# Kernel optimization log

Measured on AMD Instinct MI355X. Metric: run time of the kernel, lower is better.

## Reference

```python
import jax, jax.numpy as jnp
import numpy as np

N = 50000
E = 800000
FEAT = 128
HID = 128
HEADS = 8
HEAD_DIM = HID // HEADS  # 16
NEG_SLOPE = 0.2


def _gat_layer(x, W, a_src, a_dst, b, src, dst, num_nodes):
    # x: [N, Fin]; W: [Fin, H*C]; a_src/a_dst: [H, C]; b: [H*C]
    H, C = a_src.shape
    h = (x @ W).reshape(num_nodes, H, C)               # [N,H,C]
    alpha_s = jnp.einsum('nhc,hc->nh', h, a_src)       # [N,H]
    alpha_d = jnp.einsum('nhc,hc->nh', h, a_dst)       # [N,H]
    e = jax.nn.leaky_relu(alpha_s[src] + alpha_d[dst], NEG_SLOPE)  # [E,H]
    # segment softmax over destination nodes (every node has a self-loop)
    m = jax.ops.segment_max(e, dst, num_segments=num_nodes)
    e = jnp.exp(e - m[dst])
    s = jax.ops.segment_sum(e, dst, num_segments=num_nodes)
    alpha = e / (s[dst] + 1e-16)                       # [E,H]
    msg = alpha[:, :, None] * h[src]                   # [E,H,C]
    out = jax.ops.segment_sum(msg, dst, num_segments=num_nodes)
    return out.reshape(num_nodes, H * C) + b


def setup_inputs() -> dict:
    key = jax.random.key(0)
    ks = jax.random.split(key, 12)
    x = jax.random.normal(ks[0], (N, FEAT), dtype=jnp.float32)
    edge_index = jax.random.randint(ks[1], (2, E), 0, N, dtype=jnp.int32)
    glorot = lambda k, shape: jax.random.uniform(
        k, shape, jnp.float32,
        -jnp.sqrt(6.0 / (shape[-2] + shape[-1])),
        jnp.sqrt(6.0 / (shape[-2] + shape[-1])))
    W1 = glorot(ks[2], (FEAT, HID))
    a_src1 = glorot(ks[3], (HEADS, HEAD_DIM))
    a_dst1 = glorot(ks[4], (HEADS, HEAD_DIM))
    b1 = jnp.zeros((HID,), jnp.float32)
    W2 = glorot(ks[5], (HID, HID))
    a_src2 = glorot(ks[6], (HEADS, HEAD_DIM))
    a_dst2 = glorot(ks[7], (HEADS, HEAD_DIM))
    b2 = jnp.zeros((HID,), jnp.float32)
    return {"x": x, "edge_index": edge_index,
            "W1": W1, "a_src1": a_src1, "a_dst1": a_dst1, "b1": b1,
            "W2": W2, "a_src2": a_src2, "a_dst2": a_dst2, "b2": b2}


def reference(x, edge_index, W1, a_src1, a_dst1, b1, W2, a_src2, a_dst2, b2):
    # GATConv adds self-loops to the (dense_to_sparse-derived) edge list
    loops = jnp.arange(N, dtype=edge_index.dtype)
    src = jnp.concatenate([edge_index[0], loops])
    dst = jnp.concatenate([edge_index[1], loops])
    h = _gat_layer(x, W1, a_src1, a_dst1, b1, src, dst, N)
    h = jax.nn.elu(h)
    # dropout: inference mode (training=False) -> identity
    h = _gat_layer(h, W2, a_src2, a_dst2, b2, src, dst, N)
    return jax.nn.elu(h)
```

## Files before the change

### kernel.cpp

```cpp
#include <hip/hip_runtime.h>
#include <hip/hip_fp16.h>
#include <math.h>

#define DEGMAX 64
#define CHUNK  2048
#define CAPB   6144
#define HCAP   (CAPB / 2)

typedef _Float16 half8 __attribute__((ext_vector_type(8)));
typedef float    f32x4 __attribute__((ext_vector_type(4)));

__global__ __launch_bounds__(256) void k_csr(
        const int* __restrict__ gcur, const unsigned* __restrict__ bstore,
        int N, int* __restrict__ cnt, unsigned short* __restrict__ adjt) {
    int blk = blockIdx.x;
    int b = blk >> 1, hh = blk & 1;
    int n0 = b * 256 + hh * 128;
    int nb = N - n0; if (nb > 128) nb = 128; if (nb < 0) nb = 0;
    int ecnt = gcur[b * 16]; if (ecnt > CAPB) ecnt = CAPB;
    const unsigned* bp = bstore + (size_t)b * CAPB;
    __shared__ int lcnt[128], lofs[128], wsum[2];
    __shared__ unsigned short stage[HCAP];
    int t = threadIdx.x;
    int lo = hh * 128;

    if (t < 128) lcnt[t] = 0;
    __syncthreads();
    for (int i = t; i < ecnt; i += 256) {
        int node = bp[i] >> 16;
        if ((node >> 7) == hh) atomicAdd(&lcnt[node - lo], 1);
    }
    __syncthreads();
    int mycnt = (t < 128) ? lcnt[t] : 0;
    int lane = t & 63, wv = t >> 6;
    int x = mycnt;
    #pragma unroll
    for (int d = 1; d < 64; d <<= 1) {
        int y = __shfl_up(x, d);
        if (lane >= d) x += y;
    }
    if (lane == 63 && wv < 2) wsum[wv] = x;
    __syncthreads();
    int base0 = (wv == 1) ? wsum[0] : 0;
    int myofs = base0 + x - mycnt;
    if (t < 128) lofs[t] = myofs;
    if (t < nb) cnt[n0 + t] = mycnt;
    __syncthreads();
    if (t < 128) lcnt[t] = 0;
    __syncthreads();
    for (int i = t; i < ecnt; i += 256) {
        unsigned p = bp[i];
        int node = p >> 16;
        if ((node >> 7) == hh) {
            int ln = node - lo;
            int r = atomicAdd(&lcnt[ln], 1);
            int pos = lofs[ln] + r;
            if (pos < HCAP) stage[pos] = (unsigned short)(p & 0xffffu);
        }
    }
    __syncthreads();
    for (int ln = wv; ln < 128; ln += 4) {
        int node = n0 + ln;
        if (node < N) {
            int c = lcnt[ln]; if (c > DEGMAX) c = DEGMAX;
            int p = lofs[ln] + lane;
            if (lane < c && p < HCAP)
                *(unsigned short*)((char*)adjt + (size_t)node * 128 + lane * 2) = stage[p];
        }
    }
}

__global__ void k_wcast(const float* __restrict__ W1, const float* __restrict__ as1,
                        const float* __restrict__ ad1, __half* __restrict__ Wf1,
                        const float* __restrict__ W2, const float* __restrict__ as2,
                        const float* __restrict__ ad2, __half* __restrict__ Wf2,
                        int* __restrict__ gcur) {
    int t = threadIdx.x;
    int id2 = blockIdx.x * 256 + t;
    if (id2 < 4096) gcur[id2] = 0;
    if (id2 >= 4608) return;
    int layer = id2 >= 2304 ? 1 : 0;
    const float* W  = layer ? W2  : W1;
    const float* av_s = layer ? as2 : as1;
    const float* av_d = layer ? ad2 : ad1;
    __half* Wf = layer ? Wf2 : Wf1;
    int id = id2 - layer * 2304;
    int lane = id & 63;
    int ct = (id >> 6) % 9;
    int kc = id / 576;
    int q = lane >> 4, n = lane & 15;
    #pragma unroll
    for (int j = 0; j < 8; j++) {
        int k = kc * 32 + q * 8 + j;
        float val;
        if (ct < 8) {
            val = W[(size_t)k * 128 + ct * 16 + n];
        } else {
            int h = n & 7;
            const float* a = (n < 8) ? av_s : av_d;
            float s = 0.f;
            #pragma unroll
            for (int c = 0; c < 16; c++)
                s += W[(size_t)k * 128 + h * 16 + c] * a[h * 16 + c];
            val = s;
        }
        Wf[(size_t)id * 8 + j] = __float2half(val);
    }
}

__device__ inline float4 ld4f(const float* p) { return *(const float4*)p; }

template<typename InT>
__device__ __forceinline__ void gemm_body(
        const InT* __restrict__ X, const __half* __restrict__ Wfrag,
        __half* __restrict__ H16, float* __restrict__ as_out,
        float* __restrict__ ad_out, int M, int bid) {
    __shared__ __half xls[64][136];
    int t = threadIdx.x;
    int w = t >> 6, lane = t & 63;
    int q = lane >> 4, n = lane & 15;
    int row0 = bid * 64;

    half8 bfrag[4][2];
    #pragma unroll
    for (int kc = 0; kc < 4; kc++)
        #pragma unroll
        for (int c2 = 0; c2 < 2; c2++) {
            int ct = w * 2 + c2;
            uint4 u = *(const uint4*)(Wfrag + (((size_t)(kc * 9 + ct)) * 64 + lane) * 8);
            bfrag[kc][c2] = *(half8*)&u;
        }
    half8 bfa[4];
    if (w == 0) {
        #pragma unroll
        for (int kc = 0; kc < 4; kc++) {
            uint4 u = *(const uint4*)(Wfrag + (((size_t)(kc * 9 + 8)) * 64 + lane) * 8);
            bfa[kc] = *(half8*)&u;
        }
    }

    #pragma unroll
    for (int rep = 0; rep < 8; rep++) {
        int lin = rep * 1024 + t * 4;
        int r = lin >> 7, k = lin & 127;
        int gr = row0 + r;
        uint2 u;
        if constexpr (sizeof(InT) == 4) {
            float4 v = (gr < M) ? ld4f((const float*)&X[(size_t)gr * 128 + k])
                                : make_float4(0.f, 0.f, 0.f, 0.f);
            __half2 h0 = __floats2half2_rn(v.x, v.y);
            __half2 h1 = __floats2half2_rn(v.z, v.w);
            u = make_uint2(*(unsigned*)&h0, *(unsigned*)&h1);
        } else {
            u = (gr < M) ? *(const uint2*)&X[(size_t)gr * 128 + k] : make_uint2(0, 0);
        }
        *(uint2*)&xls[r][k] = u;
    }
    __syncthreads();

    f32x4 acc[4][2], acca[4];
    #pragma unroll
    for (int rt = 0; rt < 4; rt++) {
        acc[rt][0] = (f32x4){0.f, 0.f, 0.f, 0.f};
        acc[rt][1] = (f32x4){0.f, 0.f, 0.f, 0.f};
        acca[rt]   = (f32x4){0.f, 0.f, 0.f, 0.f};
    }

    #pragma unroll
    for (int kc = 0; kc < 4; kc++)
        #pragma unroll
        for (int rt = 0; rt < 4; rt++) {
            uint4 au = *(const uint4*)&xls[rt * 16 + n][kc * 32 + q * 8];
            half8 af = *(half8*)&au;
            acc[rt][0] = __builtin_amdgcn_mfma_f32_16x16x32_f16(af, bfrag[kc][0], acc[rt][0], 0, 0, 0);
            acc[rt][1] = __builtin_amdgcn_mfma_f32_16x16x32_f16(af, bfrag[kc][1], acc[rt][1], 0, 0, 0);
            if (w == 0)
                acca[rt] = __builtin_amdgcn_mfma_f32_16x16x32_f16(af, bfa[kc], acca[rt], 0, 0, 0);
        }

    #pragma unroll
    for (int c2 = 0; c2 < 2; c2++) {
        int h = w * 2 + c2;
        #pragma unroll
        for (int rt = 0; rt < 4; rt++)
            #pragma unroll
            for (int reg = 0; reg < 4; reg++) {
                int grow = row0 + rt * 16 + q * 4 + reg;
                if (grow < M)
                    H16[(size_t)grow * 128 + h * 16 + n] = __float2half(acc[rt][c2][reg]);
            }
    }
    if (w == 0) {
        float* aout = (n < 8) ? as_out : ad_out;
        int h = n & 7;
        #pragma unroll
        for (int rt = 0; rt < 4; rt++)
            #pragma unroll
            for (int reg = 0; reg < 4; reg++) {
                int grow = row0 + rt * 16 + q * 4 + reg;
                if (grow < M) aout[grow * 8 + h] = acca[rt][reg];
            }
    }
}

__global__ __launch_bounds__(256) void k_bin_gemm(
        const float* __restrict__ X, const __half* __restrict__ Wfrag,
        __half* __restrict__ H16, float* __restrict__ as_out,
        float* __restrict__ ad_out, int M, int Gg,
        const int* __restrict__ src, const int* __restrict__ dst, int E, int K,
        int* __restrict__ gcur, unsigned* __restrict__ bstore) {
    int bid = blockIdx.x;
    if (bid < Gg) {
        gemm_body<float>(X, Wfrag, H16, as_out, ad_out, M, bid);
        return;
    }
    __shared__ int lcnt[256];
    __shared__ int gbase[256];
    int t = threadIdx.x;
    if (t < K) lcnt[t] = 0;
    __syncthreads();
    int e0 = (bid - Gg) * CHUNK;
    unsigned pk[8]; short bk[8], rk[8];
    #pragma unroll
    for (int j = 0; j < 8; j++) {
        int e = e0 + t + j * 256;
        bool v = e < E;
        int s = v ? src[e] : 0;
        int d = v ? dst[e] : 0;
        int b = d >> 8;
        pk[j] = ((unsigned)(d & 255) << 16) | (unsigned)s;
        bk[j] = (short)b;
        rk[j] = v ? (short)atomicAdd(&lcnt[b], 1) : (short)-1;
    }
    __syncthreads();
    if (t < K) gbase[t] = lcnt[t] ? atomicAdd(&gcur[t * 16], lcnt[t]) : 0;
    __syncthreads();
    #pragma unroll
    for (int j = 0; j < 8; j++) {
        if (rk[j] >= 0) {
            int b = bk[j];
            int pos = gbase[b] + rk[j];
            if (pos < CAPB) bstore[(size_t)b * CAPB + pos] = pk[j];
        }
    }
}

__global__ __launch_bounds__(256) void k_gemm_mfma_h(
        const __half* __restrict__ X, const __half* __restrict__ Wfrag,
        __half* __restrict__ H16, float* __restrict__ as_out,
        float* __restrict__ ad_out, int M) {
    gemm_body<__half>(X, Wfrag, H16, as_out, ad_out, M, blockIdx.x);
}

#define LOADB(ii, LG, HR)                                                     \
    {                                                                         \
        int e_ = (ii) + (lane >> 3);                                          \
        int se_ = __shfl(sv, (e_ < deg) ? e_ : 0);                            \
        LG = *(const float*)(asb_ + ((unsigned)se_ * 32u + alo));             \
        _Pragma("unroll")                                                     \
        for (int j_ = 0; j_ < 8; j_++) {                                      \
            int idx_ = (ii) + j_; if (idx_ >= deg) idx_ = deg - 1;            \
            int sj_ = __shfl(sv, idx_);                                       \
            HR[j_] = *(const unsigned*)(Hb_ + ((unsigned)sj_ * 256u + hlo));  \
        }                                                                     \
    }

#define COMPB(ii, LG, HR)                                                     \
    {                                                                         \
        float v_ = LG + adv;                                                  \
        v_ = v_ > 0.f ? v_ : 0.2f * v_;                                       \
        float wgt_ = ((ii) + (lane >> 3) < deg) ? __expf(v_) : 0.f;           \
        _Pragma("unroll")                                                     \
        for (int j_ = 0; j_ < 8; j_++) {                                      \
            float wj_ = __shfl(wgt_, j_ * 8 + hd);                            \
            float2 hv_ = __half22float2(*(__half2*)&HR[j_]);                  \
            ssum += wj_; ax += wj_ * hv_.x; ay += wj_ * hv_.y;                \
        }                                                                     \
    }

template<typename OutT>
__global__ __launch_bounds__(256, 4) void k_aggregate(
        const __half* __restrict__ H, const float* __restrict__ as_,
        const float* __restrict__ ad_, const int* __restrict__ cnt,
        const unsigned short* __restrict__ adjt,
        const float* __restrict__ bias, OutT* __restrict__ out, int N) {
    int wave = (int)((blockIdx.x * blockDim.x + threadIdx.x) >> 6);
    int lane = threadIdx.x & 63;
    if (wave >= N) return;
    int n = wave;
    int hd = lane >> 3;
    const char* Hb_  = (const char*)H;
    const char* asb_ = (const char*)as_;
    unsigned hlo = (unsigned)(lane * 4);
    unsigned alo = (unsigned)((lane & 7) * 4);

    unsigned svraw = *(const unsigned short*)((const char*)adjt + (unsigned)n * 128u + (unsigned)(lane * 2));
    int deg0 = cnt[n];
    float adv = *(const float*)((const char*)ad_ + (unsigned)n * 32u + alo);
    float asv = *(const float*)((const char*)as_ + (unsigned)n * 32u + (unsigned)(hd * 4));
    float adh = *(const float*)((const char*)ad_ + (unsigned)n * 32u + (unsigned)(hd * 4));
    unsigned hrs = *(const unsigned*)(Hb_ + (unsigned)n * 256u + hlo);

    int deg = deg0 > DEGMAX ? DEGMAX : deg0;
    int sv = (lane < deg) ? (int)svraw : n;

    float vs = asv + adh;
    vs = vs > 0.f ? vs : 0.2f * vs;
    float wsf = __expf(vs);
    float2 hvs = __half22float2(*(__half2*)&hrs);
    float ssum = wsf, ax = wsf * hvs.x, ay = wsf * hvs.y;

    float lg0, lg1, lg2, lg3;
    unsigned hr0[8], hr1[8], hr2[8], hr3[8];
    if (deg > 0)  LOADB(0,  lg0, hr0);
    if (deg > 8)  LOADB(8,  lg1, hr1);
    if (deg > 16) LOADB(16, lg2, hr2);
    if (deg > 24) LOADB(24, lg3, hr3);
    if (deg > 0)  COMPB(0,  lg0, hr0);
    if (deg > 8)  COMPB(8,  lg1, hr1);
    if (deg > 16) COMPB(16, lg2, hr2);
    if (deg > 24) COMPB(24, lg3, hr3);
    for (int i = 32; i < deg; i += 8) {
        float lgt; unsigned hrt[8];
        LOADB(i, lgt, hrt);
        COMPB(i, lgt, hrt);
    }

    float inv = 1.f / (ssum + 1e-16f);
    float ox = ax * inv + bias[lane * 2];
    float oy = ay * inv + bias[lane * 2 + 1];
    ox = ox > 0.f ? ox : __expf(ox) - 1.f;
    oy = oy > 0.f ? oy : __expf(oy) - 1.f;
    if constexpr (sizeof(OutT) == 2) {
        __half2 hv = __floats2half2_rn(ox, oy);
        *(__half2*)&out[(size_t)n * 128 + lane * 2] = hv;
    } else {
        *(float2*)&out[(size_t)n * 128 + lane * 2] = make_float2(ox, oy);
    }
}

static inline char* bump(char*& w, size_t bytes) {
    char* p = w;
    w += (bytes + 255) & ~(size_t)255;
    return p;
}

extern "C" void kernel_launch(void* const* d_in, const int* in_sizes, int n_in,
                              void* d_out, int out_size, void* d_ws, size_t ws_size,
                              hipStream_t stream) {
    const float* x   = (const float*)d_in[0];
    const int*   ei  = (const int*)d_in[1];
    const float* W1  = (const float*)d_in[2];
    const float* as1 = (const float*)d_in[3];
    const float* ad1 = (const float*)d_in[4];
    const float* b1  = (const float*)d_in[5];
    const float* W2  = (const float*)d_in[6];
    const float* as2 = (const float*)d_in[7];
    const float* ad2 = (const float*)d_in[8];
    const float* b2  = (const float*)d_in[9];
    float* out = (float*)d_out;

    int N = in_sizes[0] / 128;
    int E = in_sizes[1] / 2;
    const int* srcs = ei;
    const int* dsts = ei + E;
    int K = (N + 255) >> 8;
    int Gg = (N + 63) / 64;
    int Bb = (E + CHUNK - 1) / CHUNK;

    char* w = (char*)d_ws;
    int*            cnt   = (int*)           bump(w, (size_t)N * sizeof(int));
    int*            gcur  = (int*)           bump(w, 4096 * sizeof(int));
    unsigned*       bst   = (unsigned*)      bump(w, (size_t)256 * CAPB * sizeof(unsigned));
    unsigned short* adjt  = (unsigned short*)bump(w, (size_t)N * DEGMAX * sizeof(unsigned short));
    __half*         H16   = (__half*)        bump(w, (size_t)N * 128 * sizeof(__half));
    __half*         A16   = (__half*)        bump(w, (size_t)N * 128 * sizeof(__half));
    float*          asb   = (float*)         bump(w, (size_t)N * 8 * sizeof(float));
    float*          adb   = (float*)         bump(w, (size_t)N * 8 * sizeof(float));
    __half*         Wf1   = (__half*)        bump(w, 18432 * sizeof(__half));
    __half*         Wf2   = (__half*)        bump(w, 18432 * sizeof(__half));

    k_wcast<<<18, 256, 0, stream>>>(W1, as1, ad1, Wf1, W2, as2, ad2, Wf2, gcur);
    k_bin_gemm<<<Gg + Bb, 256, 0, stream>>>(x, Wf1, H16, asb, adb, N, Gg,
                                            srcs, dsts, E, K, gcur, bst);
    k_csr<<<2 * K, 256, 0, stream>>>(gcur, bst, N, cnt, adjt);
    k_aggregate<__half><<<(N + 3) / 4, 256, 0, stream>>>(H16, asb, adb, cnt, adjt, b1, A16, N);
    k_gemm_mfma_h<<<Gg, 256, 0, stream>>>(A16, Wf2, H16, asb, adb, N);
    k_aggregate<float><<<(N + 3) / 4, 256, 0, stream>>>(H16, asb, adb, cnt, adjt, b2, out, N);
}
```

Measured before the change: 217.3 us.

## Fuse CSR build into binning kernel via grid-wide atomic barrier

Removes the separate k_csr launch. The first K binning blocks now spin on a global done counter until every binning block has finished, then each builds the adjacency list for one 256-node bucket. Edges are scattered directly into adjt with LDS atomics, replacing the old prefix-scan and staging pass. This saves a kernel launch and the staging work, but relies on all waited-on blocks being co-resident or already scheduled. It also makes the order of neighbors within adjt nondeterministic.

```diff
diff --git a/kernel.cpp b/kernel.cpp
--- a/kernel.cpp
+++ b/kernel.cpp
@@ -5,70 +5,9 @@
 #define DEGMAX 64
 #define CHUNK  2048
 #define CAPB   6144
-#define HCAP   (CAPB / 2)
 
 typedef _Float16 half8 __attribute__((ext_vector_type(8)));
 typedef float    f32x4 __attribute__((ext_vector_type(4)));
-
-__global__ __launch_bounds__(256) void k_csr(
-        const int* __restrict__ gcur, const unsigned* __restrict__ bstore,
-        int N, int* __restrict__ cnt, unsigned short* __restrict__ adjt) {
-    int blk = blockIdx.x;
-    int b = blk >> 1, hh = blk & 1;
-    int n0 = b * 256 + hh * 128;
-    int nb = N - n0; if (nb > 128) nb = 128; if (nb < 0) nb = 0;
-    int ecnt = gcur[b * 16]; if (ecnt > CAPB) ecnt = CAPB;
-    const unsigned* bp = bstore + (size_t)b * CAPB;
-    __shared__ int lcnt[128], lofs[128], wsum[2];
-    __shared__ unsigned short stage[HCAP];
-    int t = threadIdx.x;
-    int lo = hh * 128;
-
-    if (t < 128) lcnt[t] = 0;
-    __syncthreads();
-    for (int i = t; i < ecnt; i += 256) {
-        int node = bp[i] >> 16;
-        if ((node >> 7) == hh) atomicAdd(&lcnt[node - lo], 1);
-    }
-    __syncthreads();
-    int mycnt = (t < 128) ? lcnt[t] : 0;
-    int lane = t & 63, wv = t >> 6;
-    int x = mycnt;
-    #pragma unroll
-    for (int d = 1; d < 64; d <<= 1) {
-        int y = __shfl_up(x, d);
-        if (lane >= d) x += y;
-    }
-    if (lane == 63 && wv < 2) wsum[wv] = x;
-    __syncthreads();
-    int base0 = (wv == 1) ? wsum[0] : 0;
-    int myofs = base0 + x - mycnt;
-    if (t < 128) lofs[t] = myofs;
-    if (t < nb) cnt[n0 + t] = mycnt;
-    __syncthreads();
-    if (t < 128) lcnt[t] = 0;
-    __syncthreads();
-    for (int i = t; i < ecnt; i += 256) {
-        unsigned p = bp[i];
-        int node = p >> 16;
-        if ((node >> 7) == hh) {
-            int ln = node - lo;
-            int r = atomicAdd(&lcnt[ln], 1);
-            int pos = lofs[ln] + r;
-            if (pos < HCAP) stage[pos] = (unsigned short)(p & 0xffffu);
-        }
-    }
-    __syncthreads();
-    for (int ln = wv; ln < 128; ln += 4) {
-        int node = n0 + ln;
-        if (node < N) {
-            int c = lcnt[ln]; if (c > DEGMAX) c = DEGMAX;
-            int p = lofs[ln] + lane;
-            if (lane < c && p < HCAP)
-                *(unsigned short*)((char*)adjt + (size_t)node * 128 + lane * 2) = stage[p];
-        }
-    }
-}
 
 __global__ void k_wcast(const float* __restrict__ W1, const float* __restrict__ as1,
                         const float* __restrict__ ad1, __half* __restrict__ Wf1,
@@ -208,7 +147,9 @@
         __half* __restrict__ H16, float* __restrict__ as_out,
         float* __restrict__ ad_out, int M, int Gg,
         const int* __restrict__ src, const int* __restrict__ dst, int E, int K,
-        int* __restrict__ gcur, unsigned* __restrict__ bstore) {
+        int* __restrict__ gcur, unsigned* __restrict__ bstore, int Bb,
+        int* __restrict__ done, int* __restrict__ cnt,
+        unsigned short* __restrict__ adjt) {
     int bid = blockIdx.x;
     if (bid < Gg) {
         gemm_body<float>(X, Wfrag, H16, as_out, ad_out, M, bid);
@@ -217,9 +158,10 @@
     __shared__ int lcnt[256];
     __shared__ int gbase[256];
     int t = threadIdx.x;
+    int bb = bid - Gg;
     if (t < K) lcnt[t] = 0;
     __syncthreads();
-    int e0 = (bid - Gg) * CHUNK;
+    int e0 = bb * CHUNK;
     unsigned pk[8]; short bk[8], rk[8];
     #pragma unroll
     for (int j = 0; j < 8; j++) {
@@ -243,6 +185,31 @@
             if (pos < CAPB) bstore[(size_t)b * CAPB + pos] = pk[j];
         }
     }
+    __syncthreads();
+    __threadfence();
+    if (t == 0) atomicAdd(done, 1);
+    if (bb >= K) return;
+    if (t == 0) {
+        while (atomicAdd(done, 0) < Bb) __builtin_amdgcn_s_sleep(8);
+    }
+    __syncthreads();
+    __threadfence();
+    int b = bb;
+    int n0 = b << 8;
+    int ecnt = atomicAdd(&gcur[b * 16], 0); if (ecnt > CAPB) ecnt = CAPB;
+    const unsigned* bp = bstore + (size_t)b * CAPB;
+    lcnt[t] = 0;
+    __syncthreads();
+    for (int i = t; i < ecnt; i += 256) {
+        unsigned p = bp[i];
+        int node = p >> 16;
+        int r = atomicAdd(&lcnt[node], 1);
+        if (r < DEGMAX)
+            adjt[((size_t)(n0 + node) << 6) + r] = (unsigned short)(p & 0xffffu);
+    }
+    __syncthreads();
+    int n = n0 + t;
+    if (n < M) cnt[n] = lcnt[t];
 }
 
 __global__ __launch_bounds__(256) void k_gemm_mfma_h(
@@ -379,11 +346,12 @@
     float*          adb   = (float*)         bump(w, (size_t)N * 8 * sizeof(float));
     __half*         Wf1   = (__half*)        bump(w, 18432 * sizeof(__half));
     __half*         Wf2   = (__half*)        bump(w, 18432 * sizeof(__half));
+    int*            done  = gcur + 3968;
 
     k_wcast<<<18, 256, 0, stream>>>(W1, as1, ad1, Wf1, W2, as2, ad2, Wf2, gcur);
     k_bin_gemm<<<Gg + Bb, 256, 0, stream>>>(x, Wf1, H16, asb, adb, N, Gg,
-                                            srcs, dsts, E, K, gcur, bst);
-    k_csr<<<2 * K, 256, 0, stream>>>(gcur, bst, N, cnt, adjt);
+                                            srcs, dsts, E, K, gcur, bst, Bb,
+                                            done, cnt, adjt);
     k_aggregate<__half><<<(N + 3) / 4, 256, 0, stream>>>(H16, asb, adb, cnt, adjt, b1, A16, N);
     k_gemm_mfma_h<<<Gg, 256, 0, stream>>>(A16, Wf2, H16, asb, adb, N);
     k_aggregate<float><<<(N + 3) / 4, 256, 0, stream>>>(H16, asb, adb, cnt, adjt, b2, out, N);
```

Measured after the change: 297.2 us. +36.8%, slower.
